# Kernel optimization log

Hardware: AMD Instinct MI355X
Metric: run time of the kernel (lower is better)

Reference implementation:

```python
import math
import jax, jax.numpy as jnp
import numpy as np

EPS = 1e-5

def lstm(x, Wih, Whh, b):
    # x: [N,T,D]; PyTorch gate order i,f,g,o; b = b_ih + b_hh combined
    N = x.shape[0]
    H = Whh.shape[1]
    gx = jnp.einsum('ntd,gd->ntg', x, Wih) + b  # [N,T,4H]
    def step(carry, g):
        h, c = carry
        z = g + h @ Whh.T
        i, f, gg, o = jnp.split(z, 4, axis=-1)
        c = jax.nn.sigmoid(f) * c + jax.nn.sigmoid(i) * jnp.tanh(gg)
        h = jax.nn.sigmoid(o) * jnp.tanh(c)
        return (h, c), h
    init = (jnp.zeros((N, H), x.dtype), jnp.zeros((N, H), x.dtype))
    (hN, _), ys = jax.lax.scan(step, init, jnp.swapaxes(gx, 0, 1))
    return jnp.swapaxes(ys, 0, 1), hN  # outputs [N,T,H], h_n [N,H]

def bilstm_layer(x, fW, fU, fb, bW, bU, bb):
    of, _ = lstm(x, fW, fU, fb)
    ob, _ = lstm(x[:, ::-1], bW, bU, bb)
    return jnp.concatenate([of, ob[:, ::-1]], axis=-1)

def layernorm(x, g, b):
    m = jnp.mean(x, -1, keepdims=True)
    v = jnp.mean((x - m) ** 2, -1, keepdims=True)
    return (x - m) * jax.lax.rsqrt(v + EPS) * g + b

def encoder_layer(src, Wq, bq, Wk, bk, Wv, bv, Wo, bo, W1, b1, W2, b2, lng, lnb):
    B, S, d = src.shape
    G, NH = 5, 5
    dk = d // NH
    # group channel shuffle (as in source)
    qs = src.reshape(B, S, G, d // G).swapaxes(-1, -2).reshape(B, S, d)
    q = qs @ Wq.T + bq
    k = q @ Wk.T + bk   # NOTE: source applies W_k/W_v to the projected query
    v = q @ Wv.T + bv
    def heads(t):
        return t.reshape(B, S, NH, dk).transpose(0, 2, 1, 3)
    qh, kh, vh = heads(q), heads(k), heads(v)
    attn = jax.nn.softmax(jnp.einsum('bhqd,bhkd->bhqk', qh, kh) / math.sqrt(dk), axis=-1)
    o = jnp.einsum('bhqk,bhkd->bhqd', attn, vh).transpose(0, 2, 1, 3).reshape(B, S, d)
    o = o @ Wo.T + bo
    src = layernorm(src + o, lng, lnb)          # dropout is identity in eval
    ff = jax.nn.relu(src @ W1.T + b1) @ W2.T + b2
    src = layernorm(src + ff, lng, lnb)         # same LayerNorm params reused
    return src, attn

def _forward(x, qWih, qWhh, qb, kWih, kWhh, kb, vWih, vWhh, vb,
             tWq, tbq, tWk, tbk, tWv, tbv, tWo, tbo, tW1, tb1, tW2, tb2, tlng, tlnb,
             l0fWih, l0fWhh, l0fb, l0bWih, l0bWhh, l0bb,
             l1fWih, l1fWhh, l1fb, l1bWih, l1bWhh, l1bb,
             fc1W, fc1b, fc2W, fc2b):
    B, T, F = x.shape
    H = qWhh.shape[1]
    # per-feature LSTMs: shared weights across features -> batch them
    xf = x.transpose(0, 2, 1).reshape(B * F, T, 1)
    _, hq = lstm(xf, qWih, qWhh, qb)   # [B*F,H]
    _, hk = lstm(xf, kWih, kWhh, kb)   # [B*F,H]
    _, hv = lstm(xf, vWih, vWhh, vb)   # [B*F,1]
    Q = hq.reshape(B, F, H)
    K = hk.reshape(B, F, H)
    V = hv.reshape(B, F)
    # b_ij = (q_i . k_j)/sqrt(H) * v_j, softmax over j
    scores = jnp.einsum('bih,bjh->bij', Q, K) / math.sqrt(H) * V[:, None, :]
    Wsm = jax.nn.softmax(scores, axis=-1)          # [B,F,F] rows indexed by i
    attn_output = jnp.einsum('btj,bij->bti', x, Wsm)  # bmm(x, softmax_b_i)
    b = Wsm.transpose(0, 2, 1)                     # stack(b_list, dim=-1)
    src = jnp.concatenate([x, attn_output], axis=-1)  # [B,T,2F]
    attns = []
    for l in range(2):
        src, a = encoder_layer(src, tWq[l], tbq[l], tWk[l], tbk[l], tWv[l], tbv[l],
                               tWo[l], tbo[l], tW1[l], tb1[l], tW2[l], tb2[l],
                               tlng[l], tlnb[l])
        attns.append(a)
    c = jnp.stack(attns)                           # [2,B,5,T,T]
    out = bilstm_layer(src, l0fWih, l0fWhh, l0fb, l0bWih, l0bWhh, l0bb)
    out = bilstm_layer(out, l1fWih, l1fWhh, l1fb, l1bWih, l1bWhh, l1bb)
    out = jax.nn.relu(out[:, -1, :])               # [B,2H]
    out = jax.nn.relu(out @ fc1W.T + fc1b)
    out = out @ fc2W.T + fc2b                      # [B,1]
    return out, b, c

def setup_inputs() -> dict:
    B, T, F, H = 16, 128, 40, 64
    d = 2 * F
    key = jax.random.key(0)
    ks = iter(jax.random.split(key, 64))
    def n(shape, fan):
        return (jax.random.normal(next(ks), shape) / math.sqrt(fan)).astype(jnp.float32)
    inp = {'x': jax.random.normal(next(ks), (B, T, F), dtype=jnp.float32)}
    # per-feature LSTMs
    inp.update(qWih=n((4 * H, 1), 1), qWhh=n((4 * H, H), H), qb=n((4 * H,), H))
    inp.update(kWih=n((4 * H, 1), 1), kWhh=n((4 * H, H), H), kb=n((4 * H,), H))
    inp.update(vWih=n((4, 1), 1), vWhh=n((4, 1), 1), vb=n((4,), 1))
    # transformer (2 layers stacked on leading axis)
    inp.update(tWq=n((2, d, d), d), tbq=n((2, d), d), tWk=n((2, d, d), d), tbk=n((2, d), d),
               tWv=n((2, d, d), d), tbv=n((2, d), d), tWo=n((2, d, d), d), tbo=n((2, d), d),
               tW1=n((2, 4 * d, d), d), tb1=n((2, 4 * d), d), tW2=n((2, d, 4 * d), 4 * d),
               tb2=n((2, d), 4 * d), tlng=jnp.ones((2, d), jnp.float32), tlnb=jnp.zeros((2, d), jnp.float32))
    # main bidirectional 2-layer LSTM
    inp.update(l0fWih=n((4 * H, d), d), l0fWhh=n((4 * H, H), H), l0fb=n((4 * H,), H),
               l0bWih=n((4 * H, d), d), l0bWhh=n((4 * H, H), H), l0bb=n((4 * H,), H),
               l1fWih=n((4 * H, 2 * H), 2 * H), l1fWhh=n((4 * H, H), H), l1fb=n((4 * H,), H),
               l1bWih=n((4 * H, 2 * H), 2 * H), l1bWhh=n((4 * H, H), H), l1bb=n((4 * H,), H))
    inp.update(fc1W=n((H, 2 * H), 2 * H), fc1b=n((H,), 2 * H), fc2W=n((1, H), H), fc2b=n((1,), H))
    return inp

def reference(x, qWih, qWhh, qb, kWih, kWhh, kb, vWih, vWhh, vb,
              tWq, tbq, tWk, tbk, tWv, tbv, tWo, tbo, tW1, tb1, tW2, tb2, tlng, tlnb,
              l0fWih, l0fWhh, l0fb, l0bWih, l0bWhh, l0bb,
              l1fWih, l1fWhh, l1fb, l1bWih, l1bWhh, l1bb,
              fc1W, fc1b, fc2W, fc2b):
    return _forward(x, qWih, qWhh, qb, kWih, kWhh, kb, vWih, vWhh, vb,
                    tWq, tbq, tWk, tbk, tWv, tbv, tWo, tbo, tW1, tb1, tW2, tb2, tlng, tlnb,
                    l0fWih, l0fWhh, l0fb, l0bWih, l0bWhh, l0bb,
                    l1fWih, l1fWhh, l1fb, l1bWih, l1bWhh, l1bb,
                    fc1W, fc1b, fc2W, fc2b)
```

## Files before the change

kernel.cpp:

```cpp
#include <hip/hip_runtime.h>

__device__ __forceinline__ float sigf(float x){ return 1.0f/(1.0f+__expf(-x)); }
__device__ __forceinline__ float tanhfast(float x){ return 1.0f - 2.0f/(__expf(2.0f*x)+1.0f); }

#define Bn 16
#define Tn 128
#define Fn 40
#define Hn 64
#define Dn 80
#define NHn 5
#define DKn 16
#define FFn 320

#define LD4(p,i) (((const float4*)(p))[i])
#define DECL8(v, p) \
  float4 v##0=LD4(p,0), v##1=LD4(p,1), v##2=LD4(p,2), v##3=LD4(p,3), \
         v##4=LD4(p,4), v##5=LD4(p,5), v##6=LD4(p,6), v##7=LD4(p,7);
#define PIN4(P) asm volatile("" : "+v"(P.x), "+v"(P.y), "+v"(P.z), "+v"(P.w));
#define PIN8(v) PIN4(v##0) PIN4(v##1) PIN4(v##2) PIN4(v##3) PIN4(v##4) PIN4(v##5) \
  PIN4(v##6) PIN4(v##7)
#define ACC8(base) \
  { const float4 h0=hb4[(base)+0]; a += h0.x*w0.x + h0.y*w0.y + h0.z*w0.z + h0.w*w0.w; } \
  { const float4 h1=hb4[(base)+1]; a += h1.x*w1.x + h1.y*w1.y + h1.z*w1.z + h1.w*w1.w; } \
  { const float4 h2=hb4[(base)+2]; a += h2.x*w2.x + h2.y*w2.y + h2.z*w2.z + h2.w*w2.w; } \
  { const float4 h3=hb4[(base)+3]; a += h3.x*w3.x + h3.y*w3.y + h3.z*w3.z + h3.w*w3.w; } \
  { const float4 h4=hb4[(base)+4]; a += h4.x*w4.x + h4.y*w4.y + h4.z*w4.z + h4.w*w4.w; } \
  { const float4 h5=hb4[(base)+5]; a += h5.x*w5.x + h5.y*w5.y + h5.z*w5.z + h5.w*w5.w; } \
  { const float4 h6=hb4[(base)+6]; a += h6.x*w6.x + h6.y*w6.y + h6.z*w6.z + h6.w*w6.w; } \
  { const float4 h7=hb4[(base)+7]; a += h7.x*w7.x + h7.y*w7.y + h7.z*w7.z + h7.w*w7.w; }

__global__ __launch_bounds__(512) void k_feat_lstm3(
    const float* __restrict__ x,
    const float* __restrict__ qWih, const float* __restrict__ qWhh, const float* __restrict__ qb,
    const float* __restrict__ kWih, const float* __restrict__ kWhh, const float* __restrict__ kb,
    const float* __restrict__ vWih, const float* __restrict__ vWhh, const float* __restrict__ vb,
    float* __restrict__ hq, float* __restrict__ hk, float* __restrict__ hv)
{
  const int blk = blockIdx.x;
  const int t = threadIdx.x;
  if (blk >= 1280){
    const int inst = (blk - 1280)*512 + t;
    if (inst >= 640) return;
    const int bi = inst/Fn, f = inst%Fn;
    const float* xp = x + bi*Tn*Fn + f;
    const float wih0=vWih[0], wih1=vWih[1], wih2=vWih[2], wih3=vWih[3];
    const float u0=vWhh[0], u1=vWhh[1], u2=vWhh[2], u3=vWhh[3];
    const float c0=vb[0], c1=vb[1], c2=vb[2], c3=vb[3];
    float h=0.f, c=0.f;
    #pragma unroll 1
    for (int tt=0;tt<Tn;++tt){
      float xt = xp[tt*Fn];
      float zi = xt*wih0 + h*u0 + c0;
      float zf = xt*wih1 + h*u1 + c1;
      float zg = xt*wih2 + h*u2 + c2;
      float zo = xt*wih3 + h*u3 + c3;
      c = sigf(zf)*c + sigf(zi)*tanhfast(zg);
      h = sigf(zo)*tanhfast(c);
    }
    hv[inst] = h;
    return;
  }
  const bool isk = blk >= 640;
  const int inst = isk ? blk-640 : blk;
  const int bi = inst/Fn, f = inst%Fn;
  const float* Whh = isk ? kWhh : qWhh;
  const float* Wih = isk ? kWih : qWih;
  const float* bia = isk ? kb  : qb;
  float* outp = isk ? hk : hq;

  const int half = t >> 8;
  const int r    = t & 255;
  DECL8(w, Whh + r*Hn + half*32);
  PIN8(w);
  const float wih0 = Wih[r];
  const float bb0  = bia[r];

  __shared__ __align__(16) float hb[Hn];
  __shared__ float pa[512];
  __shared__ float xls[Tn];

  const float* xp = x + bi*Tn*Fn + f;
  if (t < Tn) xls[t] = xp[t*Fn];
  if (t < Hn) hb[t] = 0.f;
  float c = 0.f, h = 0.f;
  __syncthreads();

  const float4* hb4 = (const float4*)hb;
  const int jbase = half*8;
  #pragma unroll 1
  for (int step=0; step<Tn; ++step){
    const float xt = xls[step];
    float a = half ? 0.f : (bb0 + xt*wih0);
    ACC8(jbase)
    pa[t] = a;
    __syncthreads();
    if (t < Hn){
      const float zi = pa[t    ] + pa[t+256];
      const float zf = pa[t+ 64] + pa[t+320];
      const float zg = pa[t+128] + pa[t+384];
      const float zo = pa[t+192] + pa[t+448];
      c = sigf(zf)*c + sigf(zi)*tanhfast(zg);
      h = sigf(zo)*tanhfast(c);
      hb[t] = h;
    }
    __syncthreads();
  }
  if (t < Hn) outp[inst*Hn + t] = h;
}

__global__ __launch_bounds__(64) void k_featattn(
    const float* __restrict__ hq, const float* __restrict__ hk, const float* __restrict__ hv,
    float* __restrict__ Wsm, float* __restrict__ out_b)
{
  const int blk = blockIdx.x;
  const int bi = blk / Fn, i = blk % Fn;
  const int j = threadIdx.x;
  __shared__ float qrow[Hn];
  qrow[j] = hq[blk*Hn + j];
  __syncthreads();
  float s = -1e30f;
  if (j < Fn){
    const float* krow = hk + (bi*Fn + j)*Hn;
    float a = 0.f;
    #pragma unroll
    for (int h2=0; h2<Hn; ++h2) a += qrow[h2]*krow[h2];
    s = a * 0.125f * hv[bi*Fn + j];
  }
  float m = s;
  #pragma unroll
  for (int off=32; off>0; off>>=1) m = fmaxf(m, __shfl_xor(m, off));
  float e = (j < Fn) ? __expf(s - m) : 0.f;
  float tot = e;
  #pragma unroll
  for (int off=32; off>0; off>>=1) tot += __shfl_xor(tot, off);
  float p = e / tot;
  if (j < Fn){
    Wsm[blk*Fn + j] = p;
    out_b[bi*(Fn*Fn) + j*Fn + i] = p;
  }
}

__global__ __launch_bounds__(128) void k_build_src(
    const float* __restrict__ x, const float* __restrict__ Wsm, float* __restrict__ src)
{
  const int blk = blockIdx.x;
  const int bi = blk / Tn;
  const int tid = threadIdx.x;
  __shared__ float xrow[Fn];
  if (tid < Fn) xrow[tid] = x[blk*Fn + tid];
  __syncthreads();
  if (tid < Fn){
    src[blk*Dn + tid] = xrow[tid];
  } else if (tid < Dn){
    const int i = tid - Fn;
    const float* wrow = Wsm + (bi*Fn + i)*Fn;
    float a = 0.f;
    #pragma unroll
    for (int j2=0;j2<Fn;++j2) a += xrow[j2]*wrow[j2];
    src[blk*Dn + tid] = a;
  }
}

__global__ __launch_bounds__(128) void k_qkv(
    const float* __restrict__ src,
    const float* __restrict__ Wq, const float* __restrict__ bq,
    const float* __restrict__ Wk, const float* __restrict__ bk,
    const float* __restrict__ Wv, const float* __restrict__ bv,
    float* __restrict__ q, float* __restrict__ k, float* __restrict__ v)
{
  const int row = blockIdx.x;
  const int t = threadIdx.x;
  __shared__ float qs[Dn];
  __shared__ float qrow[Dn];
  if (t < Dn) qs[t] = src[row*Dn + (t%5)*16 + t/5];
  __syncthreads();
  if (t < Dn){
    const float* wr = Wq + t*Dn;
    float a = bq[t];
    #pragma unroll 8
    for (int d2=0; d2<Dn; ++d2) a += qs[d2]*wr[d2];
    qrow[t] = a;
    q[row*Dn + t] = a;
  }
  __syncthreads();
  if (t < Dn){
    const float* wk = Wk + t*Dn;
    const float* wv = Wv + t*Dn;
    float ak = bk[t], av = bv[t];
    #pragma unroll 8
    for (int d2=0; d2<Dn; ++d2){ float qq = qrow[d2]; ak += qq*wk[d2]; av += qq*wv[d2]; }
    k[row*Dn + t] = ak;
    v[row*Dn + t] = av;
  }
}

__global__ __launch_bounds__(128) void k_attn(
    const float* __restrict__ q, const float* __restrict__ k, const float* __restrict__ v,
    float* __restrict__ o, float* __restrict__ c_out)
{
  const int s1 = blockIdx.x, h = blockIdx.y, bi = blockIdx.z;
  const int s2 = threadIdx.x;
  __shared__ float qf[DKn];
  __shared__ float p[Tn];
  __shared__ float pa[128];
  __shared__ float red_m[2];
  __shared__ float red_s[2];
  if (s2 < DKn) qf[s2] = q[(bi*Tn + s1)*Dn + h*DKn + s2];
  __syncthreads();
  const float* krow = k + (bi*Tn + s2)*Dn + h*DKn;
  float a = 0.f;
  #pragma unroll
  for (int d2=0; d2<DKn; ++d2) a += qf[d2]*krow[d2];
  a *= 0.25f;
  const int wv_id = s2 >> 6;
  float m = a;
  #pragma unroll
  for (int off=32; off>0; off>>=1) m = fmaxf(m, __shfl_xor(m, off));
  if ((s2 & 63) == 0) red_m[wv_id] = m;
  __syncthreads();
  m = fmaxf(red_m[0], red_m[1]);
  float e = __expf(a - m);
  float tot = e;
  #pragma unroll
  for (int off=32; off>0; off>>=1) tot += __shfl_xor(tot, off);
  if ((s2 & 63) == 0) red_s[wv_id] = tot;
  __syncthreads();
  tot = red_s[0] + red_s[1];
  float pv = e / tot;
  p[s2] = pv;
  c_out[((bi*NHn + h)*Tn + s1)*Tn + s2] = pv;
  __syncthreads();
  {
    const int d    = s2 & 15;
    const int part = s2 >> 4;
    const float* vcol = v + bi*Tn*Dn + h*DKn + d;
    float acc = 0.f;
    #pragma unroll
    for (int jj=0; jj<16; ++jj){
      const int j2 = part*16 + jj;
      acc += p[j2]*vcol[j2*Dn];
    }
    pa[s2] = acc;
  }
  __syncthreads();
  if (s2 < DKn){
    float acc = 0.f;
    #pragma unroll
    for (int k2=0; k2<8; ++k2) acc += pa[k2*16 + s2];
    o[(bi*Tn + s1)*Dn + h*DKn + s2] = acc;
  }
}

__global__ __launch_bounds__(320) void k_oln_ffln(
    const float* __restrict__ o, const float* __restrict__ Wo, const float* __restrict__ bo,
    const float* __restrict__ W1, const float* __restrict__ b1,
    const float* __restrict__ W2, const float* __restrict__ b2,
    const float* __restrict__ lng, const float* __restrict__ lnb, float* __restrict__ src)
{
  const int row = blockIdx.x;
  const int t = threadIdx.x;
  __shared__ float orow[Dn];
  __shared__ float s1row[Dn];
  __shared__ float h1[FFn];
  __shared__ float red[128];
  if (t < Dn) orow[t] = o[row*Dn + t];
  __syncthreads();
  float val = 0.f;
  if (t < Dn){
    const float* wr = Wo + t*Dn;
    float a = bo[t];
    #pragma unroll 8
    for (int d2=0; d2<Dn; ++d2) a += orow[d2]*wr[d2];
    val = a + src[row*Dn + t];
  }
  if (t < 128) red[t] = (t < Dn) ? val : 0.f;
  __syncthreads();
  for (int s=64; s>0; s>>=1){ if (t < s) red[t] += red[t+s]; __syncthreads(); }
  float mean = red[0] * (1.f/Dn);
  __syncthreads();
  if (t < 128){ float dv = (t < Dn) ? (val - mean) : 0.f; red[t] = dv*dv; }
  __syncthreads();
  for (int s=64; s>0; s>>=1){ if (t < s) red[t] += red[t+s]; __syncthreads(); }
  float rstd = rsqrtf(red[0]*(1.f/Dn) + 1e-5f);
  if (t < Dn) s1row[t] = (val - mean)*rstd*lng[t] + lnb[t];
  __syncthreads();
  {
    const float* wr = W1 + t*Dn;
    float a = b1[t];
    #pragma unroll 8
    for (int d2=0; d2<Dn; ++d2) a += s1row[d2]*wr[d2];
    h1[t] = fmaxf(a, 0.f);
  }
  __syncthreads();
  float val2 = 0.f;
  if (t < Dn){
    const float* wr = W2 + t*FFn;
    float a = b2[t];
    #pragma unroll 8
    for (int d2=0; d2<FFn; ++d2) a += h1[d2]*wr[d2];
    val2 = a + s1row[t];
  }
  if (t < 128) red[t] = (t < Dn) ? val2 : 0.f;
  __syncthreads();
  for (int s=64; s>0; s>>=1){ if (t < s) red[t] += red[t+s]; __syncthreads(); }
  mean = red[0] * (1.f/Dn);
  __syncthreads();
  if (t < 128){ float dv = (t < Dn) ? (val2 - mean) : 0.f; red[t] = dv*dv; }
  __syncthreads();
  for (int s=64; s>0; s>>=1){ if (t < s) red[t] += red[t+s]; __syncthreads(); }
  rstd = rsqrtf(red[0]*(1.f/Dn) + 1e-5f);
  if (t < Dn) src[row*Dn + t] = (val2 - mean)*rstd*lng[t] + lnb[t];
}

template<int IND>
__global__ __launch_bounds__(256) void k_gx8(
    const float* __restrict__ X,
    const float* __restrict__ WihF, const float* __restrict__ bF,
    const float* __restrict__ WihB, const float* __restrict__ bB,
    float* __restrict__ gx)
{
  const int row0 = blockIdx.x * 8;
  const int dir = blockIdx.y;
  const int g = threadIdx.x;
  __shared__ float xs[8][IND];
  #pragma unroll
  for (int rr=0; rr<8; ++rr)
    for (int d2=g; d2<IND; d2+=256) xs[rr][d2] = X[(row0+rr)*IND + d2];
  __syncthreads();
  const float* W  = dir ? WihB : WihF;
  const float* bb = dir ? bB  : bF;
  const float* wr = W + g*IND;
  float acc[8];
  const float b0 = bb[g];
  #pragma unroll
  for (int rr=0; rr<8; ++rr) acc[rr] = b0;
  #pragma unroll 4
  for (int d2=0; d2<IND; d2+=4){
    const float4 wv = *(const float4*)(wr + d2);
    #pragma unroll
    for (int rr=0; rr<8; ++rr){
      acc[rr] += xs[rr][d2]*wv.x + xs[rr][d2+1]*wv.y + xs[rr][d2+2]*wv.z + xs[rr][d2+3]*wv.w;
    }
  }
  float* gxd = gx + dir*(Bn*Tn*256);
  #pragma unroll
  for (int rr=0; rr<8; ++rr) gxd[(row0+rr)*256 + g] = acc[rr];
}

__global__ __launch_bounds__(512)
void k_bilstm_rec5(
    const float* __restrict__ gx,
    const float* __restrict__ WhhF, const float* __restrict__ WhhB,
    float* __restrict__ outp)
{
  const int n = blockIdx.x;
  const int dir = blockIdx.y;
  const int t = threadIdx.x;
  const int half = t >> 8;
  const int r    = t & 255;
  const float* Whh = dir ? WhhB : WhhF;
  DECL8(w, Whh + r*Hn + half*32);
  PIN8(w);

  __shared__ __align__(16) float hb[Hn];
  __shared__ float pa[512];
  if (t < Hn) hb[t] = 0.f;
  float c = 0.f, h = 0.f;
  __syncthreads();

  const float* gxd = gx + dir*(Bn*Tn*256) + n*Tn*256;
  const float4* hb4 = (const float4*)hb;
  const int jbase = half*8;
  const int t0 = dir ? Tn-1 : 0;
  float g0 = half ? 0.f : gxd[t0*256 + r];
  #pragma unroll 1
  for (int step=0; step<Tn; ++step){
    const int tt = dir ? (Tn-1-step) : step;
    int tn = dir ? (Tn-2-step) : (step+1);
    tn = max(0, min(Tn-1, tn));
    const float p0 = half ? 0.f : gxd[tn*256 + r];
    float a = g0;
    ACC8(jbase)
    pa[t] = a;
    __syncthreads();
    if (t < Hn){
      const float zi = pa[t    ] + pa[t+256];
      const float zf = pa[t+ 64] + pa[t+320];
      const float zg = pa[t+128] + pa[t+384];
      const float zo = pa[t+192] + pa[t+448];
      c = sigf(zf)*c + sigf(zi)*tanhfast(zg);
      h = sigf(zo)*tanhfast(c);
      hb[t] = h;
      outp[(n*Tn + tt)*128 + dir*Hn + t] = h;
    }
    __syncthreads();
    g0 = p0;
  }
}

__global__ __launch_bounds__(128) void k_final(
    const float* __restrict__ out1,
    const float* __restrict__ fc1W, const float* __restrict__ fc1b,
    const float* __restrict__ fc2W, const float* __restrict__ fc2b,
    float* __restrict__ outp)
{
  const int n = blockIdx.x;
  const int t = threadIdx.x;
  __shared__ float r[128];
  __shared__ float a1[64];
  r[t] = fmaxf(out1[(n*Tn + (Tn-1))*128 + t], 0.f);
  __syncthreads();
  if (t < 64){
    const float* wr = fc1W + t*128;
    float a = fc1b[t];
    #pragma unroll 8
    for (int d2=0; d2<128; ++d2) a += r[d2]*wr[d2];
    a1[t] = fmaxf(a, 0.f);
  }
  __syncthreads();
  if (t == 0){
    float a = fc2b[0];
    #pragma unroll 8
    for (int d2=0; d2<64; ++d2) a += a1[d2]*fc2W[d2];
    outp[n] = a;
  }
}

extern "C" void kernel_launch(void* const* d_in, const int* in_sizes, int n_in,
                              void* d_out, int out_size, void* d_ws, size_t ws_size,
                              hipStream_t stream)
{
  const float* x     = (const float*)d_in[0];
  const float* qWih  = (const float*)d_in[1];
  const float* qWhh  = (const float*)d_in[2];
  const float* qb    = (const float*)d_in[3];
  const float* kWih  = (const float*)d_in[4];
  const float* kWhh  = (const float*)d_in[5];
  const float* kb    = (const float*)d_in[6];
  const float* vWih  = (const float*)d_in[7];
  const float* vWhh  = (const float*)d_in[8];
  const float* vb    = (const float*)d_in[9];
  const float* tWq   = (const float*)d_in[10];
  const float* tbq   = (const float*)d_in[11];
  const float* tWk   = (const float*)d_in[12];
  const float* tbk   = (const float*)d_in[13];
  const float* tWv   = (const float*)d_in[14];
  const float* tbv   = (const float*)d_in[15];
  const float* tWo   = (const float*)d_in[16];
  const float* tbo   = (const float*)d_in[17];
  const float* tW1   = (const float*)d_in[18];
  const float* tb1   = (const float*)d_in[19];
  const float* tW2   = (const float*)d_in[20];
  const float* tb2   = (const float*)d_in[21];
  const float* tlng  = (const float*)d_in[22];
  const float* tlnb  = (const float*)d_in[23];
  const float* l0fWih= (const float*)d_in[24];
  const float* l0fWhh= (const float*)d_in[25];
  const float* l0fb  = (const float*)d_in[26];
  const float* l0bWih= (const float*)d_in[27];
  const float* l0bWhh= (const float*)d_in[28];
  const float* l0bb  = (const float*)d_in[29];
  const float* l1fWih= (const float*)d_in[30];
  const float* l1fWhh= (const float*)d_in[31];
  const float* l1fb  = (const float*)d_in[32];
  const float* l1bWih= (const float*)d_in[33];
  const float* l1bWhh= (const float*)d_in[34];
  const float* l1bb  = (const float*)d_in[35];
  const float* fc1W  = (const float*)d_in[36];
  const float* fc1b  = (const float*)d_in[37];
  const float* fc2W  = (const float*)d_in[38];
  const float* fc2b  = (const float*)d_in[39];

  float* ws  = (float*)d_ws;
  float* hq  = ws;
  float* hk  = hq  + 640*64;
  float* hv  = hk  + 640*64;
  float* Wsm = hv  + 640;
  float* src = Wsm + 16*40*40;
  float* q   = src + 16*128*80;
  float* k   = q   + 16*128*80;
  float* v   = k   + 16*128*80;
  float* o   = v   + 16*128*80;
  float* gx  = o   + 16*128*80;
  float* lout0 = gx + 2*16*128*256;
  float* lout1 = lout0 + 16*128*128;

  float* outp  = (float*)d_out;
  float* out_b = outp + 16;
  float* out_c = out_b + 16*40*40;

  k_feat_lstm3<<<1282, 512, 0, stream>>>(x, qWih,qWhh,qb, kWih,kWhh,kb, vWih,vWhh,vb, hq,hk,hv);
  k_featattn<<<640, 64, 0, stream>>>(hq, hk, hv, Wsm, out_b);
  k_build_src<<<2048, 128, 0, stream>>>(x, Wsm, src);
  for (int l=0; l<2; ++l){
    k_qkv<<<2048, 128, 0, stream>>>(src, tWq + l*Dn*Dn, tbq + l*Dn,
                                    tWk + l*Dn*Dn, tbk + l*Dn,
                                    tWv + l*Dn*Dn, tbv + l*Dn, q, k, v);
    k_attn<<<dim3(128,5,16), 128, 0, stream>>>(q, k, v, o, out_c + (size_t)l*16*5*128*128);
    k_oln_ffln<<<2048, 320, 0, stream>>>(o, tWo + l*Dn*Dn, tbo + l*Dn,
                                         tW1 + l*FFn*Dn, tb1 + l*FFn,
                                         tW2 + l*Dn*FFn, tb2 + l*Dn,
                                         tlng + l*Dn, tlnb + l*Dn, src);
  }
  k_gx8<80><<<dim3(256,2), 256, 0, stream>>>(src, l0fWih, l0fb, l0bWih, l0bb, gx);
  k_bilstm_rec5<<<dim3(16,2), 512, 0, stream>>>(gx, l0fWhh, l0bWhh, lout0);
  k_gx8<128><<<dim3(256,2), 256, 0, stream>>>(lout0, l1fWih, l1fb, l1bWih, l1bb, gx);
  k_bilstm_rec5<<<dim3(16,2), 512, 0, stream>>>(gx, l1fWhh, l1bWhh, lout1);
  k_final<<<16, 128, 0, stream>>>(lout1, fc1W, fc1b, fc2W, fc2b, outp);
}
```

Before: 708.9 us.

## Split LSTM recurrence across 4-lane quads with shuffle reduction and distributed gate math

Reworks the thread-to-work mapping in the feature LSTM and bidirectional LSTM recurrence kernels. Each quad of four lanes now computes two gate rows over a quarter of the hidden vector each and reduces with wave shuffles instead of a 512-entry shared partial array. The second thread group applies tanh and sigmoid to the g and o gates and passes them through small shared arrays, so the cell update reads fewer shared values and runs across 256 lanes instead of 64. The goal is to shorten the serial per-step critical path, at the cost of extra shuffles and redundant gate math in lanes 1-3 of each quad.

```diff
diff --git a/kernel.cpp b/kernel.cpp
--- a/kernel.cpp
+++ b/kernel.cpp
@@ -13,23 +13,14 @@
 #define FFn 320
 
 #define LD4(p,i) (((const float4*)(p))[i])
-#define DECL8(v, p) \
-  float4 v##0=LD4(p,0), v##1=LD4(p,1), v##2=LD4(p,2), v##3=LD4(p,3), \
-         v##4=LD4(p,4), v##5=LD4(p,5), v##6=LD4(p,6), v##7=LD4(p,7);
 #define PIN4(P) asm volatile("" : "+v"(P.x), "+v"(P.y), "+v"(P.z), "+v"(P.w));
-#define PIN8(v) PIN4(v##0) PIN4(v##1) PIN4(v##2) PIN4(v##3) PIN4(v##4) PIN4(v##5) \
-  PIN4(v##6) PIN4(v##7)
-#define ACC8(base) \
-  { const float4 h0=hb4[(base)+0]; a += h0.x*w0.x + h0.y*w0.y + h0.z*w0.z + h0.w*w0.w; } \
-  { const float4 h1=hb4[(base)+1]; a += h1.x*w1.x + h1.y*w1.y + h1.z*w1.z + h1.w*w1.w; } \
-  { const float4 h2=hb4[(base)+2]; a += h2.x*w2.x + h2.y*w2.y + h2.z*w2.z + h2.w*w2.w; } \
-  { const float4 h3=hb4[(base)+3]; a += h3.x*w3.x + h3.y*w3.y + h3.z*w3.z + h3.w*w3.w; } \
-  { const float4 h4=hb4[(base)+4]; a += h4.x*w4.x + h4.y*w4.y + h4.z*w4.z + h4.w*w4.w; } \
-  { const float4 h5=hb4[(base)+5]; a += h5.x*w5.x + h5.y*w5.y + h5.z*w5.z + h5.w*w5.w; } \
-  { const float4 h6=hb4[(base)+6]; a += h6.x*w6.x + h6.y*w6.y + h6.z*w6.z + h6.w*w6.w; } \
-  { const float4 h7=hb4[(base)+7]; a += h7.x*w7.x + h7.y*w7.y + h7.z*w7.z + h7.w*w7.w; }
-
-__global__ __launch_bounds__(512) void k_feat_lstm3(
+#define DECL4(v, p) \
+  float4 v##0=LD4(p,0), v##1=LD4(p,1), v##2=LD4(p,2), v##3=LD4(p,3);
+#define PINQ(v) PIN4(v##0) PIN4(v##1) PIN4(v##2) PIN4(v##3)
+#define DOT4(acc, W_, H_) acc += (H_).x*(W_).x + (H_).y*(W_).y + (H_).z*(W_).z + (H_).w*(W_).w;
+
+
+__global__ __launch_bounds__(512) void k_feat_lstm7(
     const float* __restrict__ x,
     const float* __restrict__ qWih, const float* __restrict__ qWhh, const float* __restrict__ qb,
     const float* __restrict__ kWih, const float* __restrict__ kWhh, const float* __restrict__ kb,
@@ -68,44 +59,52 @@
   const float* bia = isk ? kb  : qb;
   float* outp = isk ? hk : hq;
 
-  const int half = t >> 8;
-  const int r    = t & 255;
-  DECL8(w, Whh + r*Hn + half*32);
-  PIN8(w);
-  const float wih0 = Wih[r];
-  const float bb0  = bia[r];
+  const int gp = t >> 8;
+  const int r  = (t & 255) >> 2;
+  const int q  = t & 3;
+  const int rA = r + gp*128;
+  const int rB = rA + 64;
+  DECL4(wa, Whh + rA*Hn + q*16);
+  DECL4(wb, Whh + rB*Hn + q*16);
+  PINQ(wa); PINQ(wb);
+  const float wihA = Wih[rA], wihB = Wih[rB];
+  const float bbA  = bia[rA], bbB  = bia[rB];
 
   __shared__ __align__(16) float hb[Hn];
-  __shared__ float pa[512];
+  __shared__ float ex0[Hn], ex1[Hn];
   __shared__ float xls[Tn];
 
-  const float* xp = x + bi*Tn*Fn + f;
-  if (t < Tn) xls[t] = xp[t*Fn];
+  if (t < Tn) xls[t] = x[(bi*Tn + t)*Fn + f];
   if (t < Hn) hb[t] = 0.f;
   float c = 0.f, h = 0.f;
   __syncthreads();
 
   const float4* hb4 = (const float4*)hb;
-  const int jbase = half*8;
+  const int q4 = q*4;
   #pragma unroll 1
   for (int step=0; step<Tn; ++step){
     const float xt = xls[step];
-    float a = half ? 0.f : (bb0 + xt*wih0);
-    ACC8(jbase)
-    pa[t] = a;
+    float aA = (q==0) ? (bbA + xt*wihA) : 0.f;
+    float aB = (q==0) ? (bbB + xt*wihB) : 0.f;
+    {
+      const float4 h0=hb4[q4+0], h1=hb4[q4+1], h2=hb4[q4+2], h3=hb4[q4+3];
+      DOT4(aA, wa0, h0) DOT4(aB, wb0, h0)
+      DOT4(aA, wa1, h1) DOT4(aB, wb1, h1)
+      DOT4(aA, wa2, h2) DOT4(aB, wb2, h2)
+      DOT4(aA, wa3, h3) DOT4(aB, wb3, h3)
+    }
+    aA += __shfl_xor(aA, 1); aA += __shfl_xor(aA, 2);
+    aB += __shfl_xor(aB, 1); aB += __shfl_xor(aB, 2);
+    if (gp && q==0){ ex0[r] = tanhfast(aA); ex1[r] = sigf(aB); }
     __syncthreads();
-    if (t < Hn){
-      const float zi = pa[t    ] + pa[t+256];
-      const float zf = pa[t+ 64] + pa[t+320];
-      const float zg = pa[t+128] + pa[t+384];
-      const float zo = pa[t+192] + pa[t+448];
-      c = sigf(zf)*c + sigf(zi)*tanhfast(zg);
-      h = sigf(zo)*tanhfast(c);
-      hb[t] = h;
+    if (!gp){
+      c = sigf(aB)*c + sigf(aA)*ex0[r];
+      h = ex1[r]*tanhfast(c);
+      if (q==0) hb[r] = h;
     }
     __syncthreads();
   }
-  if (t < Hn) outp[inst*Hn + t] = h;
+  if (!gp && q==0) outp[inst*Hn + r] = h;
 }
 
 __global__ __launch_bounds__(64) void k_featattn(
@@ -348,7 +347,7 @@
 }
 
 __global__ __launch_bounds__(512)
-void k_bilstm_rec5(
+void k_bilstm_rec6(
     const float* __restrict__ gx,
     const float* __restrict__ WhhF, const float* __restrict__ WhhB,
     float* __restrict__ outp)
@@ -356,45 +355,57 @@
   const int n = blockIdx.x;
   const int dir = blockIdx.y;
   const int t = threadIdx.x;
-  const int half = t >> 8;
-  const int r    = t & 255;
+  const int gp = t >> 8;
+  const int r  = (t & 255) >> 2;
+  const int q  = t & 3;
+  const int rA = r + gp*128;
+  const int rB = rA + 64;
   const float* Whh = dir ? WhhB : WhhF;
-  DECL8(w, Whh + r*Hn + half*32);
-  PIN8(w);
+  DECL4(wa, Whh + rA*Hn + q*16);
+  DECL4(wb, Whh + rB*Hn + q*16);
+  PINQ(wa); PINQ(wb);
 
   __shared__ __align__(16) float hb[Hn];
-  __shared__ float pa[512];
+  __shared__ float ex0[Hn], ex1[Hn];
   if (t < Hn) hb[t] = 0.f;
   float c = 0.f, h = 0.f;
   __syncthreads();
 
   const float* gxd = gx + dir*(Bn*Tn*256) + n*Tn*256;
   const float4* hb4 = (const float4*)hb;
-  const int jbase = half*8;
+  const int q4 = q*4;
   const int t0 = dir ? Tn-1 : 0;
-  float g0 = half ? 0.f : gxd[t0*256 + r];
+  float gA = (q==0) ? gxd[t0*256 + rA] : 0.f;
+  float gB = (q==0) ? gxd[t0*256 + rB] : 0.f;
   #pragma unroll 1
   for (int step=0; step<Tn; ++step){
     const int tt = dir ? (Tn-1-step) : step;
     int tn = dir ? (Tn-2-step) : (step+1);
     tn = max(0, min(Tn-1, tn));
-    const float p0 = half ? 0.f : gxd[tn*256 + r];
-    float a = g0;
-    ACC8(jbase)
-    pa[t] = a;
+    const float pA = (q==0) ? gxd[tn*256 + rA] : 0.f;
+    const float pB = (q==0) ? gxd[tn*256 + rB] : 0.f;
+    float aA = gA, aB = gB;
+    {
+      const float4 h0=hb4[q4+0], h1=hb4[q4+1], h2=hb4[q4+2], h3=hb4[q4+3];
+      DOT4(aA, wa0, h0) DOT4(aB, wb0, h0)
+      DOT4(aA, wa1, h1) DOT4(aB, wb1, h1)
+      DOT4(aA, wa2, h2) DOT4(aB, wb2, h2)
+      DOT4(aA, wa3, h3) DOT4(aB, wb3, h3)
+    }
+    aA += __shfl_xor(aA, 1); aA += __shfl_xor(aA, 2);
+    aB += __shfl_xor(aB, 1); aB += __shfl_xor(aB, 2);
+    if (gp && q==0){ ex0[r] = tanhfast(aA); ex1[r] = sigf(aB); }
     __syncthreads();
-    if (t < Hn){
-      const float zi = pa[t    ] + pa[t+256];
-      const float zf = pa[t+ 64] + pa[t+320];
-      const float zg = pa[t+128] + pa[t+384];
-      const float zo = pa[t+192] + pa[t+448];
-      c = sigf(zf)*c + sigf(zi)*tanhfast(zg);
-      h = sigf(zo)*tanhfast(c);
-      hb[t] = h;
-      outp[(n*Tn + tt)*128 + dir*Hn + t] = h;
+    if (!gp){
+      c = sigf(aB)*c + sigf(aA)*ex0[r];
+      h = ex1[r]*tanhfast(c);
+      if (q==0){
+        hb[r] = h;
+        outp[(n*Tn + tt)*128 + dir*Hn + r] = h;
+      }
     }
     __syncthreads();
-    g0 = p0;
+    gA = pA; gB = pB;
   }
 }
 
@@ -489,7 +500,7 @@
   float* out_b = outp + 16;
   float* out_c = out_b + 16*40*40;
 
-  k_feat_lstm3<<<1282, 512, 0, stream>>>(x, qWih,qWhh,qb, kWih,kWhh,kb, vWih,vWhh,vb, hq,hk,hv);
+  k_feat_lstm7<<<1282, 512, 0, stream>>>(x, qWih,qWhh,qb, kWih,kWhh,kb, vWih,vWhh,vb, hq,hk,hv);
   k_featattn<<<640, 64, 0, stream>>>(hq, hk, hv, Wsm, out_b);
   k_build_src<<<2048, 128, 0, stream>>>(x, Wsm, src);
   for (int l=0; l<2; ++l){
@@ -503,8 +514,8 @@
                                          tlng + l*Dn, tlnb + l*Dn, src);
   }
   k_gx8<80><<<dim3(256,2), 256, 0, stream>>>(src, l0fWih, l0fb, l0bWih, l0bb, gx);
-  k_bilstm_rec5<<<dim3(16,2), 512, 0, stream>>>(gx, l0fWhh, l0bWhh, lout0);
+  k_bilstm_rec6<<<dim3(16,2), 512, 0, stream>>>(gx, l0fWhh, l0bWhh, lout0);
   k_gx8<128><<<dim3(256,2), 256, 0, stream>>>(lout0, l1fWih, l1fb, l1bWih, l1bb, gx);
-  k_bilstm_rec5<<<dim3(16,2), 512, 0, stream>>>(gx, l1fWhh, l1bWhh, lout1);
+  k_bilstm_rec6<<<dim3(16,2), 512, 0, stream>>>(gx, l1fWhh, l1bWhh, lout1);
   k_final<<<16, 128, 0, stream>>>(lout1, fc1W, fc1b, fc2W, fc2b, outp);
 }
```

Result: slower. 761.0 us (+7.4%).
